# Optimization experiments

Measured on AMD Instinct MI355X. Metric: run time of the kernel, lower is better.

Reference implementation:

```python
import jax, jax.numpy as jnp
import numpy as np

B, C, H, W = 16, 192, 56, 56
WS = 7; L = WS * WS; NH = 8; HD = C // NH
SHIFTS = (0, 3, 0, 3)  # shift = 0 if i%2==0 else window_size//2


def _ln(x, g, b):
    m = jnp.mean(x, -1, keepdims=True)
    v = jnp.var(x, -1, keepdims=True)
    return (x - m) * jax.lax.rsqrt(v + 1e-5) * g + b


def _win_part(x):
    # (b, H, W, c) -> (b*nW, L, c)
    b, c = x.shape[0], x.shape[-1]
    x = x.reshape(b, H // WS, WS, W // WS, WS, c).transpose(0, 1, 3, 2, 4, 5)
    return x.reshape(-1, L, c)


def _win_rev(xw, b):
    # (b*nW, L, c) -> (b, H, W, c)
    c = xw.shape[-1]
    x = xw.reshape(b, H // WS, W // WS, WS, WS, c).transpose(0, 1, 3, 2, 4, 5)
    return x.reshape(b, H, W, c)


def _rel_index():
    co = np.stack(np.meshgrid(np.arange(WS), np.arange(WS), indexing='ij')).reshape(2, -1)
    r = (co[:, :, None] - co[:, None, :]).transpose(1, 2, 0).astype(np.int64)
    r[..., 0] += WS - 1; r[..., 1] += WS - 1; r[..., 0] *= 2 * WS - 1
    return r.sum(-1)  # (L, L)

REL_IDX = _rel_index()


def _mask(shift):
    if shift == 0:
        return None
    img = np.zeros((1, H, W, 1), np.float32)
    cnt = 0.0
    sl = (slice(0, H - WS), slice(H - WS, H - shift), slice(H - shift, None))
    for hs in sl:
        for ws_ in sl:
            img[:, hs, ws_, :] = cnt
            cnt += 1.0
    mw = np.asarray(_win_part(jnp.asarray(img))).reshape(-1, L)
    am = mw[:, None, :] - mw[:, :, None]
    return jnp.asarray(np.where(am != 0, -100.0, 0.0).astype(np.float32))  # (nW, L, L)

MASKS = [_mask(s) for s in SHIFTS]


def _block(x, n1g, n1b, qw, qb, pw, pb, tab, n2g, n2b, f1w, f1b, f2w, f2b, shift, mask):
    b = x.shape[0]
    sc = x
    x = _ln(x, n1g, n1b)
    if shift:
        x = jnp.roll(x, (-shift, -shift), (1, 2))
    xw = _win_part(x)  # (b*nW, L, C)
    qkv = (xw @ qw.T + qb).reshape(-1, L, 3, NH, HD).transpose(2, 0, 3, 1, 4)
    q, k, v = qkv[0], qkv[1], qkv[2]  # (nB, NH, L, HD)
    attn = jnp.einsum('bhid,bhjd->bhij', q * (HD ** -0.5), k)
    attn = attn + tab[REL_IDX].transpose(2, 0, 1)  # relative position bias (NH, L, L)
    if mask is not None:
        nW = mask.shape[0]
        attn = (attn.reshape(b, nW, NH, L, L) + mask[None, :, None]).reshape(-1, NH, L, L)
    attn = jax.nn.softmax(attn, -1)
    out = jnp.einsum('bhij,bhjd->bhid', attn, v).transpose(0, 2, 1, 3).reshape(-1, L, C)
    out = out @ pw.T + pb
    x = _win_rev(out, b)
    if shift:
        x = jnp.roll(x, (shift, shift), (1, 2))
    x = sc + x
    y = _ln(x, n2g, n2b)
    y = jax.nn.gelu(y @ f1w.T + f1b, approximate=False) @ f2w.T + f2b
    return x + y


def _conv_bn_relu(x, w, b, g, bt, m, v):
    x = jax.lax.conv_general_dilated(x, w, (1, 1), ((1, 1), (1, 1)),
                                     dimension_numbers=('NCHW', 'OIHW', 'NCHW'))
    x = x + b[None, :, None, None]
    x = (x - m[None, :, None, None]) * jax.lax.rsqrt(v + 1e-5)[None, :, None, None]
    x = x * g[None, :, None, None] + bt[None, :, None, None]
    return jax.nn.relu(x)


def setup_inputs() -> dict:
    key = jax.random.key(0)
    ks = iter(jax.random.split(key, 48))
    rn = lambda shape, s=0.02: jax.random.normal(next(ks), shape, jnp.float32) * s
    OD = 96
    return dict(
        x=jax.random.normal(next(ks), (B, C, H, W), jnp.float32),
        pos_embed=rn((1, H * W, C)),
        proj_w=rn((C, C)), proj_b=jnp.zeros((C,)),
        pe_g=jnp.ones((C,)), pe_b=jnp.zeros((C,)),
        n1_g=jnp.ones((4, C)), n1_b=jnp.zeros((4, C)),
        qkv_w=rn((4, 3 * C, C)), qkv_b=jnp.zeros((4, 3 * C)),
        attn_pw=rn((4, C, C)), attn_pb=jnp.zeros((4, C)),
        rel_tab=rn((4, (2 * WS - 1) ** 2, NH)),
        n2_g=jnp.ones((4, C)), n2_b=jnp.zeros((4, C)),
        fc1_w=rn((4, 4 * C, C)), fc1_b=jnp.zeros((4, 4 * C)),
        fc2_w=rn((4, C, 4 * C)), fc2_b=jnp.zeros((4, C)),
        c1_w=rn((C, C, 3, 3)), c1_b=jnp.zeros((C,)),
        bn1_g=jnp.ones((C,)), bn1_b=jnp.zeros((C,)), bn1_m=rn((C,), 0.1), bn1_v=jnp.ones((C,)),
        c2_w=rn((OD, C, 3, 3)), c2_b=jnp.zeros((OD,)),
        bn2_g=jnp.ones((OD,)), bn2_b=jnp.zeros((OD,)), bn2_m=rn((OD,), 0.1), bn2_v=jnp.ones((OD,)),
    )


def reference(x, pos_embed, proj_w, proj_b, pe_g, pe_b, n1_g, n1_b, qkv_w, qkv_b,
              attn_pw, attn_pb, rel_tab, n2_g, n2_b, fc1_w, fc1_b, fc2_w, fc2_b,
              c1_w, c1_b, bn1_g, bn1_b, bn1_m, bn1_v,
              c2_w, c2_b, bn2_g, bn2_b, bn2_m, bn2_v):
    # PatchEmbedding: 1x1 conv == per-pixel linear, then LN, + pos embed
    t = jnp.einsum('bchw,dc->bhwd', x, proj_w) + proj_b  # (B, H, W, D)
    t = _ln(t.reshape(B, H * W, C), pe_g, pe_b) + pos_embed
    o = t.reshape(B, H, W, C)
    for i in range(4):
        o = _block(o, n1_g[i], n1_b[i], qkv_w[i], qkv_b[i], attn_pw[i], attn_pb[i],
                   rel_tab[i], n2_g[i], n2_b[i], fc1_w[i], fc1_b[i], fc2_w[i], fc2_b[i],
                   SHIFTS[i], MASKS[i])
    ds2 = o.transpose(0, 3, 1, 2)  # (B, C, H, W)
    h1 = _conv_bn_relu(ds2, c1_w, c1_b, bn1_g, bn1_b, bn1_m, bn1_v)
    conv_out = _conv_bn_relu(h1, c2_w, c2_b, bn2_g, bn2_b, bn2_m, bn2_v)
    return (conv_out, ds2)
```

## Files before the change

kernel.cpp:

```cpp
#include <hip/hip_runtime.h>
#include <math.h>

typedef unsigned short u16;
typedef unsigned int u32;
typedef __attribute__((ext_vector_type(8))) short short8;
typedef __attribute__((ext_vector_type(4))) float f32x4;

#define IMG 56
#define HW_ 3136
#define NTOK 50176
#define C_DIM 192
#define CONV_OUT_SZ 4816896

#define SZ_QKV (4*576*192)
#define SZ_FC1 (4*768*192)
#define SZ_FC2 (4*192*768)
#define SZ_PW  (4*192*192)
#define SZ_PROJ (192*192)
#define SZ_C1R (192*1728)
#define SZ_C2R (128*1728)

__device__ inline float bf2f(u16 v) {
  u32 u = ((u32)v) << 16; float f; __builtin_memcpy(&f, &u, 4); return f;
}
__device__ inline u16 f2bf(float f) {
  u32 u; __builtin_memcpy(&u, &f, 4);
  u += 0x7FFF + ((u >> 16) & 1);
  return (u16)(u >> 16);
}
__device__ inline void glds16(const u16* g, u16* l) {
  __builtin_amdgcn_global_load_lds((const __attribute__((address_space(1))) u32*)g,
                                   (__attribute__((address_space(3))) u32*)l, 16, 0, 0);
}
__device__ inline u32 pk_bf16(float a, float b) {
  u32 r;
  asm("v_cvt_pk_bf16_f32 %0, %1, %2" : "=v"(r) : "v"(a), "v"(b));
  return r;
}

template<int AMODE, int EPI>
__global__ __launch_bounds__(256) void gmm(
    const u16* __restrict__ A, const u16* __restrict__ W,
    const float* __restrict__ bias, void* __restrict__ Cout,
    int M, int N, int K,
    const float* __restrict__ bg, const float* __restrict__ bb,
    const float* __restrict__ bm, const float* __restrict__ bv, int shiftp)
{
  __shared__ u16 As[128 * 64];
  __shared__ u16 Bs[64 * 64];
  const int tid = threadIdx.x;
  const int m0 = blockIdx.x * 128, n0 = blockIdx.y * 64;
  const int lane = tid & 63, wid = tid >> 6;
  const int wm = (wid >> 1) * 64, wn = (wid & 1) * 32;
  const int fr = lane & 15, fg = lane >> 4;
  f32x4 acc[4][2] = {};

  for (int kc = 0; kc < K; kc += 64) {
    #pragma unroll
    for (int it = 0; it < 2; ++it) {
      const int g = it * 256 + tid;
      const int row = g >> 3, cb = (g & 7) << 4;
      const int sc = cb ^ ((row & 7) << 4);
      glds16(W + (size_t)(n0 + row) * K + kc + (sc >> 1), Bs + g * 8);
    }
    if (AMODE == 0) {
      #pragma unroll
      for (int it = 0; it < 4; ++it) {
        const int g = it * 256 + tid;
        const int row = g >> 3, cb = (g & 7) << 4;
        const int sc = cb ^ ((row & 7) << 4);
        glds16(A + (size_t)(m0 + row) * K + kc + (sc >> 1), As + g * 8);
      }
    } else {
      #pragma unroll
      for (int it = 0; it < 4; ++it) {
        const int g = it * 256 + tid;
        const int row = g >> 3, cb = (g & 7) << 4;
        const int m = m0 + row;
        const int b = m / HW_, pp = m - b * HW_;
        const int y = pp / IMG, x = pp - (pp / IMG) * IMG;
        const int kg = kc + (cb >> 1);
        const int s = kg / C_DIM, ic = kg - s * C_DIM;
        const int yy = y + s / 3 - 1, xx = x + (s % 3) - 1;
        short8 v = {0, 0, 0, 0, 0, 0, 0, 0};
        if ((unsigned)yy < IMG && (unsigned)xx < IMG)
          v = *(const short8*)(A + ((size_t)(b * HW_ + yy * IMG + xx)) * C_DIM + ic);
        *(short8*)(As + row * 64 + ((cb ^ ((row & 7) << 4)) >> 1)) = v;
      }
    }
    __syncthreads();
    #pragma unroll
    for (int ks = 0; ks < 2; ++ks) {
      const int kb = ks * 64 + fg * 16;
      short8 af[4], bfv[2];
      #pragma unroll
      for (int i = 0; i < 4; ++i) {
        const int row = wm + i * 16 + fr;
        af[i] = *(const short8*)(As + ((row * 128 + (kb ^ ((row & 7) << 4))) >> 1));
      }
      #pragma unroll
      for (int j = 0; j < 2; ++j) {
        const int row = wn + j * 16 + fr;
        bfv[j] = *(const short8*)(Bs + ((row * 128 + (kb ^ ((row & 7) << 4))) >> 1));
      }
      #pragma unroll
      for (int i = 0; i < 4; ++i)
        #pragma unroll
        for (int j = 0; j < 2; ++j)
          acc[i][j] = __builtin_amdgcn_mfma_f32_16x16x32_bf16(af[i], bfv[j], acc[i][j], 0, 0, 0);
    }
    __syncthreads();
  }

  const int c0 = n0 + wn + fr;
  const int c1i = (EPI == 4) ? min(c0 + 16, N - 1) : (c0 + 16);
  const float bias0 = bias[c0], bias1 = bias[c1i];
  float s0 = 0.f, h0 = 0.f, s1 = 0.f, h1 = 0.f;
  if (EPI == 3 || EPI == 4) {
    s0 = bg[c0] * rsqrtf(bv[c0] + 1e-5f); h0 = bb[c0] - bm[c0] * s0;
    s1 = bg[c1i] * rsqrtf(bv[c1i] + 1e-5f); h1 = bb[c1i] - bm[c1i] * s1;
  }

  if (EPI == 0 || EPI == 1 || EPI == 3) {
    #pragma unroll
    for (int i = 0; i < 4; ++i) {
      #pragma unroll
      for (int r = 0; r < 4; ++r) {
        const int ml = wm + i * 16 + fg * 4 + r;
        #pragma unroll
        for (int j = 0; j < 2; ++j) {
          float v = acc[i][j][r] + (j ? bias1 : bias0);
          if (EPI == 1) v = 0.5f * v * (1.f + erff(v * 0.70710678118f));
          if (EPI == 3) { v = v * (j ? s1 : s0) + (j ? h1 : h0); v = fmaxf(v, 0.f); }
          const int cl = wn + j * 16 + fr;
          As[ml * 64 + ((cl & 7) | ((((cl >> 3) ^ ml) & 7) << 3))] = f2bf(v);
        }
      }
    }
    __syncthreads();
    #pragma unroll
    for (int p = 0; p < 4; ++p) {
      const int id = p * 256 + tid;
      const int ml = id >> 3, g = id & 7;
      const int pg = (g ^ ml) & 7;
      *(short8*)((u16*)Cout + (size_t)(m0 + ml) * N + n0 + g * 8) =
          *(const short8*)(As + ml * 64 + pg * 8);
    }
  } else {
    #pragma unroll
    for (int i = 0; i < 4; ++i) {
      #pragma unroll
      for (int r = 0; r < 4; ++r) {
        const int m = m0 + wm + i * 16 + fg * 4 + r;
        size_t sbase = 0;
        if (EPI == 6) {
          const int wno = m / 49, within = m - wno * 49;
          const int b2 = wno >> 6, wb3 = wno & 63;
          const int wr = within / 7, wc = within - wr * 7;
          int y2 = (wb3 >> 3) * 7 + wr + shiftp; if (y2 >= IMG) y2 -= IMG;
          int x2 = (wb3 & 7) * 7 + wc + shiftp; if (x2 >= IMG) x2 -= IMG;
          sbase = ((size_t)(b2 * HW_ + y2 * IMG + x2)) * C_DIM;
        }
        #pragma unroll
        for (int j = 0; j < 2; ++j) {
          const int c = c0 + j * 16;
          float v = acc[i][j][r] + (j ? bias1 : bias0);
          if (EPI == 4) { v = v * (j ? s1 : s0) + (j ? h1 : h0); v = fmaxf(v, 0.f); }
          if (EPI == 5) {
            ((float*)Cout)[(size_t)m * N + c] = v;
          } else if (EPI == 2) {
            ((float*)Cout)[(size_t)m * N + c] += v;
          } else if (EPI == 6) {
            ((float*)Cout)[sbase + c] += v;
          } else {
            if (c < N) {
              const int b = m / HW_, pp = m - b * HW_;
              ((float*)Cout)[((size_t)b * N + c) * HW_ + pp] = v;
            }
          }
        }
      }
    }
  }
}

__device__ inline void stv(float* p, float v) { *p = v; }
__device__ inline void stv(u16* p, float v) { *p = f2bf(v); }

template<typename OT>
__global__ __launch_bounds__(256) void ln_k(
    const float* __restrict__ in, OT* __restrict__ outp,
    const float* __restrict__ g, const float* __restrict__ bta,
    const float* __restrict__ pos, int winpart, int shift)
{
  const int t = blockIdx.x * 4 + (threadIdx.x >> 6);
  const int lane = threadIdx.x & 63;
  const float* xr = in + (size_t)t * C_DIM;
  const float v0 = xr[lane], v1 = xr[lane + 64], v2 = xr[lane + 128];
  float s = v0 + v1 + v2;
  float ss = v0 * v0 + v1 * v1 + v2 * v2;
  #pragma unroll
  for (int off = 32; off > 0; off >>= 1) {
    s += __shfl_xor(s, off);
    ss += __shfl_xor(ss, off);
  }
  const float mean = s * (1.f / 192.f);
  const float inv = rsqrtf(ss * (1.f / 192.f) - mean * mean + 1e-5f);
  const int b = t / HW_, pp = t - b * HW_;
  size_t obase;
  if (winpart) {
    const int y = pp / IMG, x = pp - (pp / IMG) * IMG;
    int yr = y - shift; if (yr < 0) yr += IMG;
    int xs = x - shift; if (xs < 0) xs += IMG;
    const int win = b * 64 + (yr / 7) * 8 + (xs / 7);
    const int within = (yr % 7) * 7 + (xs % 7);
    obase = ((size_t)win * 49 + within) * C_DIM;
  } else {
    obase = (size_t)t * C_DIM;
  }
  OT* o = outp + obase;
  float p0 = 0.f, p1 = 0.f, p2 = 0.f;
  if (pos) {
    const float* pr = pos + (size_t)pp * C_DIM;
    p0 = pr[lane]; p1 = pr[lane + 64]; p2 = pr[lane + 128];
  }
  stv(o + lane,       (v0 - mean) * inv * g[lane]       + bta[lane]       + p0);
  stv(o + lane + 64,  (v1 - mean) * inv * g[lane + 64]  + bta[lane + 64]  + p1);
  stv(o + lane + 128, (v2 - mean) * inv * g[lane + 128] + bta[lane + 128] + p2);
}

template<int SHIFT>
__global__ __launch_bounds__(256) void attn_m(
    const u16* __restrict__ qkv, u16* __restrict__ outp,
    const float* __restrict__ rel)
{
  __shared__ u16 VT[128 * 64];
  __shared__ float relS[4 * 176 + 16];
  const int tid = threadIdx.x;
  const int wid = tid >> 6, lane = tid & 63;
  const int fr = lane & 15, fg = lane >> 4;
  const int win = blockIdx.x >> 1;
  const int hb = blockIdx.x & 1;
  const int h = hb * 4 + wid;
  const u16* wbase = qkv + (size_t)win * 49 * 576;

  {
    u32* vz = (u32*)VT;
    #pragma unroll
    for (int it = 0; it < 16; ++it) vz[it * 256 + tid] = 0;
  }
  for (int id = tid; id < 169 * 4; id += 256) {
    const int hl = id & 3, ridx = id >> 2;
    relS[hl * 176 + ridx] = rel[ridx * 8 + hb * 4 + hl];
  }
  __syncthreads();
  for (int id = tid; id < 49 * 24; id += 256) {
    const int j = id / 24, dq = id - (id / 24) * 24;
    const int dd = dq * 4;
    const uint2 v = *(const uint2*)(wbase + j * 576 + 384 + hb * 96 + dd);
    const u16* pv = (const u16*)&v;
    const int wpr = dd / 24, dl = dd - wpr * 24;
    #pragma unroll
    for (int e = 0; e < 4; ++e) {
      const int row = wpr * 32 + dl + e;
      VT[(row * 128 + ((j * 2) ^ (((row >> 2) & 7) << 4))) >> 1] = pv[e];
    }
  }
  __syncthreads();

  short8 qf[4], kf[4];
  #pragma unroll
  for (int t = 0; t < 4; ++t) {
    const int row = t * 16 + fr;
    if (fg < 3) {
      qf[t] = *(const short8*)(wbase + row * 576 + h * 24 + fg * 8);
      kf[t] = *(const short8*)(wbase + row * 576 + 192 + h * 24 + fg * 8);
    } else {
      qf[t] = (short8){0, 0, 0, 0, 0, 0, 0, 0};
      kf[t] = (short8){0, 0, 0, 0, 0, 0, 0, 0};
    }
  }

  short8 av[2][2];
  #pragma unroll
  for (int db = 0; db < 2; ++db) {
    const int row = wid * 32 + db * 16 + fr;
    const int swz = ((row >> 2) & 7) << 4;
    #pragma unroll
    for (int ks = 0; ks < 2; ++ks) {
      const uint2 lo = *(const uint2*)((const char*)VT + row * 128 + (((2 * ks) * 32 + fg * 8) ^ swz));
      const uint2 hi = *(const uint2*)((const char*)VT + row * 128 + (((2 * ks + 1) * 32 + fg * 8) ^ swz));
      u32 w[4] = {lo.x, lo.y, hi.x, hi.y};
      av[db][ks] = *(short8*)w;
    }
  }

  const int wb2 = win & 63;
  const int hblk = wb2 >> 3, wblk = wb2 & 7;

  u32 joffPk[4];
  u32 jregPk[2] = {0, 0};
  #pragma unroll
  for (int nj = 0; nj < 4; ++nj) {
    u32 w = 0;
    #pragma unroll
    for (int r = 0; r < 4; ++r) {
      const int j = nj * 16 + fg * 4 + r;
      const int r2 = j / 7, c2 = j - r2 * 7;
      w |= (u32)(r2 * 13 + c2) << (r * 8);
      if (SHIFT) {
        const int hj = hblk * 7 + r2, wj = wblk * 7 + c2;
        const int rj = (hj < 49 ? 0 : (hj < 53 ? 1 : 2)) * 3 + (wj < 49 ? 0 : (wj < 53 ? 1 : 2));
        jregPk[nj >> 1] |= (u32)rj << (((nj & 1) * 4 + r) * 4);
      }
    }
    joffPk[nj] = w;
  }

  const float* relw = relS + wid * 176;
  const float scl = 0.20412414523193154f;

  #pragma unroll
  for (int mi = 0; mi < 4; ++mi) {
    f32x4 sacc[4];
    #pragma unroll
    for (int nj = 0; nj < 4; ++nj)
      sacc[nj] = __builtin_amdgcn_mfma_f32_16x16x32_bf16(kf[nj], qf[mi],
                                                         (f32x4){0, 0, 0, 0}, 0, 0, 0);
    const int i = mi * 16 + fr;
    const int r1 = i / 7, c1 = i - r1 * 7;
    const int base13 = (r1 + 6) * 13 + (c1 + 6);
    int ri = 0;
    if (SHIFT) {
      const int hi2 = hblk * 7 + r1, wi2 = wblk * 7 + c1;
      ri = (hi2 < 49 ? 0 : (hi2 < 53 ? 1 : 2)) * 3 + (wi2 < 49 ? 0 : (wi2 < 53 ? 1 : 2));
    }
    float p[16];
    float mx = -1e30f;
    #pragma unroll
    for (int nj = 0; nj < 4; ++nj) {
      #pragma unroll
      for (int r = 0; r < 4; ++r) {
        const int j = nj * 16 + fg * 4 + r;
        int idx = base13 - (int)((joffPk[nj] >> (r * 8)) & 0xff);
        idx = min(max(idx, 0), 168);
        float v = sacc[nj][r] * scl + relw[idx];
        if (SHIFT) {
          const int rj = (jregPk[nj >> 1] >> (((nj & 1) * 4 + r) * 4)) & 0xf;
          v = (ri != rj) ? v - 100.f : v;
        }
        v = (j < 49) ? v : -1e30f;
        p[nj * 4 + r] = v;
        mx = fmaxf(mx, v);
      }
    }
    mx = fmaxf(mx, __shfl_xor(mx, 16));
    mx = fmaxf(mx, __shfl_xor(mx, 32));
    float sum = 0.f;
    #pragma unroll
    for (int e = 0; e < 16; ++e) { p[e] = __expf(p[e] - mx); sum += p[e]; }
    sum += __shfl_xor(sum, 16);
    sum += __shfl_xor(sum, 32);
    const float inv = 1.f / sum;
    short8 pb[2];
    #pragma unroll
    for (int ks = 0; ks < 2; ++ks) {
      u32 w[4];
      #pragma unroll
      for (int half = 0; half < 2; ++half) {
        const int nj = 2 * ks + half;
        w[half * 2 + 0] = pk_bf16(p[nj * 4 + 0] * inv, p[nj * 4 + 1] * inv);
        w[half * 2 + 1] = pk_bf16(p[nj * 4 + 2] * inv, p[nj * 4 + 3] * inv);
      }
      pb[ks] = *(short8*)w;
    }
    f32x4 o0 = {0, 0, 0, 0}, o1 = {0, 0, 0, 0};
    o0 = __builtin_amdgcn_mfma_f32_16x16x32_bf16(av[0][0], pb[0], o0, 0, 0, 0);
    o0 = __builtin_amdgcn_mfma_f32_16x16x32_bf16(av[0][1], pb[1], o0, 0, 0, 0);
    o1 = __builtin_amdgcn_mfma_f32_16x16x32_bf16(av[1][0], pb[0], o1, 0, 0, 0);
    o1 = __builtin_amdgcn_mfma_f32_16x16x32_bf16(av[1][1], pb[1], o1, 0, 0, 0);
    if (i < 49) {
      u16* orow = outp + ((size_t)win * 49 + i) * C_DIM + h * 24;
      *(uint2*)(orow + fg * 4) =
          make_uint2(pk_bf16(o0[0], o0[1]), pk_bf16(o0[2], o0[3]));
      if (fg < 2)
        *(uint2*)(orow + 16 + fg * 4) =
            make_uint2(pk_bf16(o1[0], o1[1]), pk_bf16(o1[2], o1[3]));
    }
  }
}

__global__ __launch_bounds__(256) void transpose_k(
    const float* __restrict__ in, float* __restrict__ outp)
{
  __shared__ float tile[32][33];
  const int p0 = blockIdx.x * 32;
  const int c0 = blockIdx.y * 32;
  const int tid = threadIdx.x;
  #pragma unroll
  for (int it = 0; it < 4; ++it) {
    const int id = tid + it * 256;
    const int r = id >> 5, cc = id & 31;
    tile[r][cc] = in[(size_t)(p0 + r) * C_DIM + c0 + cc];
  }
  __syncthreads();
  const int b = p0 / HW_, pp0 = p0 - b * HW_;
  #pragma unroll
  for (int it = 0; it < 4; ++it) {
    const int id = tid + it * 256;
    const int cl = id >> 5, pl = id & 31;
    outp[((size_t)b * C_DIM + c0 + cl) * HW_ + pp0 + pl] = tile[pl][cl];
  }
}

__global__ __launch_bounds__(256) void tok_k(
    const float* __restrict__ in, u16* __restrict__ outp)
{
  __shared__ float tile[32][33];
  const int t0 = blockIdx.x * 32;
  const int c0 = blockIdx.y * 32;
  const int tid = threadIdx.x;
  const int b = t0 / HW_, p0 = t0 - b * HW_;
  #pragma unroll
  for (int it = 0; it < 4; ++it) {
    const int id = tid + it * 256;
    const int cl = id >> 5, pl = id & 31;
    tile[cl][pl] = in[((size_t)b * C_DIM + c0 + cl) * HW_ + p0 + pl];
  }
  __syncthreads();
  #pragma unroll
  for (int it = 0; it < 4; ++it) {
    const int id = tid + it * 256;
    const int r = id >> 5, cc = id & 31;
    outp[(size_t)(t0 + r) * C_DIM + c0 + cc] = f2bf(tile[cc][r]);
  }
}

__global__ __launch_bounds__(256) void cvt_k(
    const float* __restrict__ in, u16* __restrict__ outp, int n4)
{
  const int i = blockIdx.x * 256 + threadIdx.x;
  if (i >= n4) return;
  const float4 v = ((const float4*)in)[i];
  u32 lo = (u32)f2bf(v.x) | ((u32)f2bf(v.y) << 16);
  u32 hi = (u32)f2bf(v.z) | ((u32)f2bf(v.w) << 16);
  ((uint2*)outp)[i] = make_uint2(lo, hi);
}

__global__ __launch_bounds__(256) void cvtall_k(
    const float* __restrict__ qkv_w, const float* __restrict__ fc1_w,
    const float* __restrict__ fc2_w, const float* __restrict__ attn_pw,
    const float* __restrict__ proj_w, const float* __restrict__ c1_w,
    const float* __restrict__ c2_w, u16* __restrict__ wbf)
{
  const int i = blockIdx.x * 256 + threadIdx.x;
  const int off1 = SZ_QKV, off2 = off1 + SZ_FC1, off3 = off2 + SZ_FC2,
            off4 = off3 + SZ_PW, off5 = off4 + SZ_PROJ, off6 = off5 + SZ_C1R,
            off7 = off6 + SZ_C2R;
  if (i >= off7) return;
  float v;
  if (i < off1) v = qkv_w[i];
  else if (i < off2) v = fc1_w[i - off1];
  else if (i < off3) v = fc2_w[i - off2];
  else if (i < off4) v = attn_pw[i - off3];
  else if (i < off5) v = proj_w[i - off4];
  else if (i < off6) {
    const int e = i - off5;
    const int n = e / 1728, kkk = e - n * 1728;
    const int s = kkk / C_DIM, ic = kkk - s * C_DIM;
    v = c1_w[((size_t)n * C_DIM + ic) * 9 + s];
  } else {
    const int e = i - off6;
    const int n = e / 1728, kkk = e - n * 1728;
    const int s = kkk / C_DIM, ic = kkk - s * C_DIM;
    v = (n < 96) ? c2_w[((size_t)n * C_DIM + ic) * 9 + s] : 0.f;
  }
  wbf[i] = f2bf(v);
}

extern "C" void kernel_launch(void* const* d_in, const int* in_sizes, int n_in,
                              void* d_out, int out_size, void* d_ws, size_t ws_size,
                              hipStream_t stream)
{
  const float* x       = (const float*)d_in[0];
  const float* pos     = (const float*)d_in[1];
  const float* proj_w  = (const float*)d_in[2];
  const float* proj_b  = (const float*)d_in[3];
  const float* pe_g    = (const float*)d_in[4];
  const float* pe_b    = (const float*)d_in[5];
  const float* n1_g    = (const float*)d_in[6];
  const float* n1_b    = (const float*)d_in[7];
  const float* qkv_w   = (const float*)d_in[8];
  const float* qkv_b   = (const float*)d_in[9];
  const float* attn_pw = (const float*)d_in[10];
  const float* attn_pb = (const float*)d_in[11];
  const float* rel_tab = (const float*)d_in[12];
  const float* n2_g    = (const float*)d_in[13];
  const float* n2_b    = (const float*)d_in[14];
  const float* fc1_w   = (const float*)d_in[15];
  const float* fc1_b   = (const float*)d_in[16];
  const float* fc2_w   = (const float*)d_in[17];
  const float* fc2_b   = (const float*)d_in[18];
  const float* c1_w    = (const float*)d_in[19];
  const float* c1_b    = (const float*)d_in[20];
  const float* bn1_g   = (const float*)d_in[21];
  const float* bn1_b   = (const float*)d_in[22];
  const float* bn1_m   = (const float*)d_in[23];
  const float* bn1_v   = (const float*)d_in[24];
  const float* c2_w    = (const float*)d_in[25];
  const float* c2_b    = (const float*)d_in[26];
  const float* bn2_g   = (const float*)d_in[27];
  const float* bn2_b   = (const float*)d_in[28];
  const float* bn2_m   = (const float*)d_in[29];
  const float* bn2_v   = (const float*)d_in[30];
  float* out = (float*)d_out;

  const size_t BUF  = (size_t)NTOK * C_DIM * 4;
  const size_t BIGB = (size_t)NTOK * 576 * 2;
  char* ws = (char*)d_ws;
  float* act   = (float*)ws;
  u16*   big16 = (u16*)(ws + BUF);
  float* big32 = (float*)(ws + BUF);
  u16*   xln   = (u16*)(ws + BUF + BIGB);
  u16* attn_out = (u16*)d_out;
  u16* wbf = (u16*)((char*)d_out + (size_t)CONV_OUT_SZ * 4);

  const size_t O_QKV = 0;
  const size_t O_FC1 = O_QKV + SZ_QKV;
  const size_t O_FC2 = O_FC1 + SZ_FC1;
  const size_t O_PW  = O_FC2 + SZ_FC2;
  const size_t O_PROJ= O_PW  + SZ_PW;
  const size_t O_C1  = O_PROJ+ SZ_PROJ;
  const size_t O_C2  = O_C1  + SZ_C1R;

  const dim3 blk(256);

  const int cvtall_n = SZ_QKV + SZ_FC1 + SZ_FC2 + SZ_PW + SZ_PROJ + SZ_C1R + SZ_C2R;
  cvtall_k<<<(cvtall_n + 255) / 256, blk, 0, stream>>>(
      qkv_w, fc1_w, fc2_w, attn_pw, proj_w, c1_w, c2_w, wbf);

  tok_k<<<dim3(1568, 6), blk, 0, stream>>>(x, xln);
  gmm<0, 5><<<dim3(392, 3), blk, 0, stream>>>(
      xln, wbf + O_PROJ, proj_b, big32, NTOK, 192, 192,
      nullptr, nullptr, nullptr, nullptr, 0);
  ln_k<float><<<12544, blk, 0, stream>>>(big32, act, pe_g, pe_b, pos, 0, 0);

  for (int i = 0; i < 4; ++i) {
    const int shift = (i & 1) ? 3 : 0;
    ln_k<u16><<<12544, blk, 0, stream>>>(act, xln, n1_g + i * 192, n1_b + i * 192,
                                         nullptr, 1, shift);
    gmm<0, 0><<<dim3(392, 9), blk, 0, stream>>>(
        xln, wbf + O_QKV + (size_t)i * 576 * 192, qkv_b + i * 576, big16,
        NTOK, 576, 192, nullptr, nullptr, nullptr, nullptr, 0);
    if (shift)
      attn_m<3><<<2048, blk, 0, stream>>>(big16, attn_out, rel_tab + i * 169 * 8);
    else
      attn_m<0><<<2048, blk, 0, stream>>>(big16, attn_out, rel_tab + i * 169 * 8);
    gmm<0, 6><<<dim3(392, 3), blk, 0, stream>>>(
        attn_out, wbf + O_PW + (size_t)i * 192 * 192, attn_pb + i * 192, act,
        NTOK, 192, 192, nullptr, nullptr, nullptr, nullptr, shift);
    ln_k<u16><<<12544, blk, 0, stream>>>(act, xln, n2_g + i * 192, n2_b + i * 192,
                                         nullptr, 0, 0);
    for (int c = 0; c < 2; ++c) {
      gmm<0, 1><<<dim3(196, 12), blk, 0, stream>>>(
          xln + (size_t)c * 25088 * 192, wbf + O_FC1 + (size_t)i * 768 * 192,
          fc1_b + i * 768, big16, 25088, 768, 192,
          nullptr, nullptr, nullptr, nullptr, 0);
      gmm<0, 2><<<dim3(196, 3), blk, 0, stream>>>(
          big16, wbf + O_FC2 + (size_t)i * 192 * 768, fc2_b + i * 192,
          act + (size_t)c * 25088 * 192, 25088, 192, 768,
          nullptr, nullptr, nullptr, nullptr, 0);
    }
  }

  cvt_k<<<(NTOK * C_DIM / 4 + 255)/256, blk, 0, stream>>>(act, xln, NTOK * C_DIM / 4);
  gmm<1, 3><<<dim3(392, 3), blk, 0, stream>>>(
      xln, wbf + O_C1, c1_b, big16, NTOK, 192, 1728, bn1_g, bn1_b, bn1_m, bn1_v, 0);
  gmm<1, 4><<<dim3(392, 2), blk, 0, stream>>>(
      big16, wbf + O_C2, c2_b, out, NTOK, 96, 1728, bn2_g, bn2_b, bn2_m, bn2_v, 0);
  transpose_k<<<dim3(1568, 6), blk, 0, stream>>>(act, out + CONV_OUT_SZ);
}
```

Baseline: 962.3 us.

## Enlarge GEMM tile to 256x64 with each wave covering 64x64

The shared GEMM kernel's M tile grows from 128 to 256 rows. Each of the four waves now computes a 64x64 sub-tile (4x4 MFMA accumulators) instead of 64x32, so every B fragment loaded from LDS is reused across more MFMAs and the grid size is halved. The implicit-im2col conv loader is also split into batches of four global loads before the LDS stores, to put more loads in flight. In exchange the kernel uses more registers and LDS (which may lower occupancy) and launches fewer blocks, which may underfill the GPU for the smaller GEMMs.

```diff
diff --git a/kernel.cpp b/kernel.cpp
--- a/kernel.cpp
+++ b/kernel.cpp
@@ -46,14 +46,14 @@
     const float* __restrict__ bg, const float* __restrict__ bb,
     const float* __restrict__ bm, const float* __restrict__ bv, int shiftp)
 {
-  __shared__ u16 As[128 * 64];
+  __shared__ u16 As[256 * 64];
   __shared__ u16 Bs[64 * 64];
   const int tid = threadIdx.x;
-  const int m0 = blockIdx.x * 128, n0 = blockIdx.y * 64;
+  const int m0 = blockIdx.x * 256, n0 = blockIdx.y * 64;
   const int lane = tid & 63, wid = tid >> 6;
-  const int wm = (wid >> 1) * 64, wn = (wid & 1) * 32;
+  const int wm = wid * 64;
   const int fr = lane & 15, fg = lane >> 4;
-  f32x4 acc[4][2] = {};
+  f32x4 acc[4][4] = {};
 
   for (int kc = 0; kc < K; kc += 64) {
     #pragma unroll
@@ -65,7 +65,7 @@
     }
     if (AMODE == 0) {
       #pragma unroll
-      for (int it = 0; it < 4; ++it) {
+      for (int it = 0; it < 8; ++it) {
         const int g = it * 256 + tid;
         const int row = g >> 3, cb = (g & 7) << 4;
         const int sc = cb ^ ((row & 7) << 4);
@@ -73,52 +73,65 @@
       }
     } else {
       #pragma unroll
-      for (int it = 0; it < 4; ++it) {
-        const int g = it * 256 + tid;
-        const int row = g >> 3, cb = (g & 7) << 4;
-        const int m = m0 + row;
-        const int b = m / HW_, pp = m - b * HW_;
-        const int y = pp / IMG, x = pp - (pp / IMG) * IMG;
-        const int kg = kc + (cb >> 1);
-        const int s = kg / C_DIM, ic = kg - s * C_DIM;
-        const int yy = y + s / 3 - 1, xx = x + (s % 3) - 1;
-        short8 v = {0, 0, 0, 0, 0, 0, 0, 0};
-        if ((unsigned)yy < IMG && (unsigned)xx < IMG)
-          v = *(const short8*)(A + ((size_t)(b * HW_ + yy * IMG + xx)) * C_DIM + ic);
-        *(short8*)(As + row * 64 + ((cb ^ ((row & 7) << 4)) >> 1)) = v;
+      for (int half = 0; half < 2; ++half) {
+        short8 cst[4];
+        #pragma unroll
+        for (int it = 0; it < 4; ++it) {
+          const int g = (half * 4 + it) * 256 + tid;
+          const int row = g >> 3, cb = (g & 7) << 4;
+          const int m = m0 + row;
+          const int b = m / HW_, pp = m - b * HW_;
+          const int y = pp / IMG, x = pp - (pp / IMG) * IMG;
+          const int kg = kc + (cb >> 1);
+          const int s = kg / C_DIM, ic = kg - s * C_DIM;
+          const int yy = y + s / 3 - 1, xx = x + (s % 3) - 1;
+          short8 v = {0, 0, 0, 0, 0, 0, 0, 0};
+          if ((unsigned)yy < IMG && (unsigned)xx < IMG)
+            v = *(const short8*)(A + ((size_t)(b * HW_ + yy * IMG + xx)) * C_DIM + ic);
+          cst[it] = v;
+        }
+        #pragma unroll
+        for (int it = 0; it < 4; ++it) {
+          const int g = (half * 4 + it) * 256 + tid;
+          const int row = g >> 3, cb = (g & 7) << 4;
+          *(short8*)(As + row * 64 + ((cb ^ ((row & 7) << 4)) >> 1)) = cst[it];
+        }
       }
     }
     __syncthreads();
     #pragma unroll
     for (int ks = 0; ks < 2; ++ks) {
       const int kb = ks * 64 + fg * 16;
-      short8 af[4], bfv[2];
+      short8 af[4], bfv[4];
       #pragma unroll
       for (int i = 0; i < 4; ++i) {
         const int row = wm + i * 16 + fr;
         af[i] = *(const short8*)(As + ((row * 128 + (kb ^ ((row & 7) << 4))) >> 1));
       }
       #pragma unroll
-      for (int j = 0; j < 2; ++j) {
-        const int row = wn + j * 16 + fr;
+      for (int j = 0; j < 4; ++j) {
+        const int row = j * 16 + fr;
         bfv[j] = *(const short8*)(Bs + ((row * 128 + (kb ^ ((row & 7) << 4))) >> 1));
       }
       #pragma unroll
       for (int i = 0; i < 4; ++i)
         #pragma unroll
-        for (int j = 0; j < 2; ++j)
+        for (int j = 0; j < 4; ++j)
           acc[i][j] = __builtin_amdgcn_mfma_f32_16x16x32_bf16(af[i], bfv[j], acc[i][j], 0, 0, 0);
     }
     __syncthreads();
   }
 
-  const int c0 = n0 + wn + fr;
-  const int c1i = (EPI == 4) ? min(c0 + 16, N - 1) : (c0 + 16);
-  const float bias0 = bias[c0], bias1 = bias[c1i];
-  float s0 = 0.f, h0 = 0.f, s1 = 0.f, h1 = 0.f;
-  if (EPI == 3 || EPI == 4) {
-    s0 = bg[c0] * rsqrtf(bv[c0] + 1e-5f); h0 = bb[c0] - bm[c0] * s0;
-    s1 = bg[c1i] * rsqrtf(bv[c1i] + 1e-5f); h1 = bb[c1i] - bm[c1i] * s1;
+  const int c0 = n0 + fr;
+  float bias_[4], sc_[4], hh_[4];
+  #pragma unroll
+  for (int j = 0; j < 4; ++j) {
+    const int cj = (EPI == 4) ? min(c0 + j * 16, N - 1) : (c0 + j * 16);
+    bias_[j] = bias[cj];
+    if (EPI == 3 || EPI == 4) {
+      sc_[j] = bg[cj] * rsqrtf(bv[cj] + 1e-5f);
+      hh_[j] = bb[cj] - bm[cj] * sc_[j];
+    }
   }
 
   if (EPI == 0 || EPI == 1 || EPI == 3) {
@@ -128,18 +141,18 @@
       for (int r = 0; r < 4; ++r) {
         const int ml = wm + i * 16 + fg * 4 + r;
         #pragma unroll
-        for (int j = 0; j < 2; ++j) {
-          float v = acc[i][j][r] + (j ? bias1 : bias0);
+        for (int j = 0; j < 4; ++j) {
+          float v = acc[i][j][r] + bias_[j];
           if (EPI == 1) v = 0.5f * v * (1.f + erff(v * 0.70710678118f));
-          if (EPI == 3) { v = v * (j ? s1 : s0) + (j ? h1 : h0); v = fmaxf(v, 0.f); }
-          const int cl = wn + j * 16 + fr;
+          if (EPI == 3) { v = v * sc_[j] + hh_[j]; v = fmaxf(v, 0.f); }
+          const int cl = j * 16 + fr;
           As[ml * 64 + ((cl & 7) | ((((cl >> 3) ^ ml) & 7) << 3))] = f2bf(v);
         }
       }
     }
     __syncthreads();
     #pragma unroll
-    for (int p = 0; p < 4; ++p) {
+    for (int p = 0; p < 8; ++p) {
       const int id = p * 256 + tid;
       const int ml = id >> 3, g = id & 7;
       const int pg = (g ^ ml) & 7;
@@ -162,10 +175,10 @@
           sbase = ((size_t)(b2 * HW_ + y2 * IMG + x2)) * C_DIM;
         }
         #pragma unroll
-        for (int j = 0; j < 2; ++j) {
+        for (int j = 0; j < 4; ++j) {
           const int c = c0 + j * 16;
-          float v = acc[i][j][r] + (j ? bias1 : bias0);
-          if (EPI == 4) { v = v * (j ? s1 : s0) + (j ? h1 : h0); v = fmaxf(v, 0.f); }
+          float v = acc[i][j][r] + bias_[j];
+          if (EPI == 4) { v = v * sc_[j] + hh_[j]; v = fmaxf(v, 0.f); }
           if (EPI == 5) {
             ((float*)Cout)[(size_t)m * N + c] = v;
           } else if (EPI == 2) {
@@ -540,7 +553,7 @@
       qkv_w, fc1_w, fc2_w, attn_pw, proj_w, c1_w, c2_w, wbf);
 
   tok_k<<<dim3(1568, 6), blk, 0, stream>>>(x, xln);
-  gmm<0, 5><<<dim3(392, 3), blk, 0, stream>>>(
+  gmm<0, 5><<<dim3(196, 3), blk, 0, stream>>>(
       xln, wbf + O_PROJ, proj_b, big32, NTOK, 192, 192,
       nullptr, nullptr, nullptr, nullptr, 0);
   ln_k<float><<<12544, blk, 0, stream>>>(big32, act, pe_g, pe_b, pos, 0, 0);
@@ -549,24 +562,24 @@
     const int shift = (i & 1) ? 3 : 0;
     ln_k<u16><<<12544, blk, 0, stream>>>(act, xln, n1_g + i * 192, n1_b + i * 192,
                                          nullptr, 1, shift);
-    gmm<0, 0><<<dim3(392, 9), blk, 0, stream>>>(
+    gmm<0, 0><<<dim3(196, 9), blk, 0, stream>>>(
         xln, wbf + O_QKV + (size_t)i * 576 * 192, qkv_b + i * 576, big16,
         NTOK, 576, 192, nullptr, nullptr, nullptr, nullptr, 0);
     if (shift)
       attn_m<3><<<2048, blk, 0, stream>>>(big16, attn_out, rel_tab + i * 169 * 8);
     else
       attn_m<0><<<2048, blk, 0, stream>>>(big16, attn_out, rel_tab + i * 169 * 8);
-    gmm<0, 6><<<dim3(392, 3), blk, 0, stream>>>(
+    gmm<0, 6><<<dim3(196, 3), blk, 0, stream>>>(
         attn_out, wbf + O_PW + (size_t)i * 192 * 192, attn_pb + i * 192, act,
         NTOK, 192, 192, nullptr, nullptr, nullptr, nullptr, shift);
     ln_k<u16><<<12544, blk, 0, stream>>>(act, xln, n2_g + i * 192, n2_b + i * 192,
                                          nullptr, 0, 0);
     for (int c = 0; c < 2; ++c) {
-      gmm<0, 1><<<dim3(196, 12), blk, 0, stream>>>(
+      gmm<0, 1><<<dim3(98, 12), blk, 0, stream>>>(
           xln + (size_t)c * 25088 * 192, wbf + O_FC1 + (size_t)i * 768 * 192,
           fc1_b + i * 768, big16, 25088, 768, 192,
           nullptr, nullptr, nullptr, nullptr, 0);
-      gmm<0, 2><<<dim3(196, 3), blk, 0, stream>>>(
+      gmm<0, 2><<<dim3(98, 3), blk, 0, stream>>>(
           big16, wbf + O_FC2 + (size_t)i * 192 * 768, fc2_b + i * 192,
           act + (size_t)c * 25088 * 192, 25088, 192, 768,
           nullptr, nullptr, nullptr, nullptr, 0);
@@ -574,9 +587,9 @@
   }
 
   cvt_k<<<(NTOK * C_DIM / 4 + 255)/256, blk, 0, stream>>>(act, xln, NTOK * C_DIM / 4);
-  gmm<1, 3><<<dim3(392, 3), blk, 0, stream>>>(
+  gmm<1, 3><<<dim3(196, 3), blk, 0, stream>>>(
       xln, wbf + O_C1, c1_b, big16, NTOK, 192, 1728, bn1_g, bn1_b, bn1_m, bn1_v, 0);
-  gmm<1, 4><<<dim3(392, 2), blk, 0, stream>>>(
+  gmm<1, 4><<<dim3(196, 2), blk, 0, stream>>>(
       big16, wbf + O_C2, c2_b, out, NTOK, 96, 1728, bn2_g, bn2_b, bn2_m, bn2_v, 0);
   transpose_k<<<dim3(1568, 6), blk, 0, stream>>>(act, out + CONV_OUT_SZ);
 }
```

Result: slower. 1.163 ms (+20.9%).

## Store residual stream in bf16 and drop LDS-staged epilogue

Applied to the files above, without the earlier changes.

The residual activation buffer changes from fp32 to bf16. GEMM epilogues now read-modify-write bf16 directly, the layernorm reads bf16 with packed loads, and the final conversion kernel is removed because the conv GEMM consumes the activation directly. The aim is to halve the memory traffic of the residual stream across the many LN and GEMM passes. In exchange, residual accumulation loses precision, which risks exceeding the tolerance. The bf16 epilogue also switches from coalesced LDS-staged vector stores to scattered 2-byte scalar stores, which may hurt write efficiency.

```diff
diff --git a/kernel.cpp b/kernel.cpp
--- a/kernel.cpp
+++ b/kernel.cpp
@@ -120,63 +120,38 @@
     s0 = bg[c0] * rsqrtf(bv[c0] + 1e-5f); h0 = bb[c0] - bm[c0] * s0;
     s1 = bg[c1i] * rsqrtf(bv[c1i] + 1e-5f); h1 = bb[c1i] - bm[c1i] * s1;
   }
-
-  if (EPI == 0 || EPI == 1 || EPI == 3) {
-    #pragma unroll
-    for (int i = 0; i < 4; ++i) {
-      #pragma unroll
-      for (int r = 0; r < 4; ++r) {
-        const int ml = wm + i * 16 + fg * 4 + r;
-        #pragma unroll
-        for (int j = 0; j < 2; ++j) {
-          float v = acc[i][j][r] + (j ? bias1 : bias0);
-          if (EPI == 1) v = 0.5f * v * (1.f + erff(v * 0.70710678118f));
-          if (EPI == 3) { v = v * (j ? s1 : s0) + (j ? h1 : h0); v = fmaxf(v, 0.f); }
-          const int cl = wn + j * 16 + fr;
-          As[ml * 64 + ((cl & 7) | ((((cl >> 3) ^ ml) & 7) << 3))] = f2bf(v);
-        }
-      }
-    }
-    __syncthreads();
-    #pragma unroll
-    for (int p = 0; p < 4; ++p) {
-      const int id = p * 256 + tid;
-      const int ml = id >> 3, g = id & 7;
-      const int pg = (g ^ ml) & 7;
-      *(short8*)((u16*)Cout + (size_t)(m0 + ml) * N + n0 + g * 8) =
-          *(const short8*)(As + ml * 64 + pg * 8);
-    }
-  } else {
-    #pragma unroll
-    for (int i = 0; i < 4; ++i) {
-      #pragma unroll
-      for (int r = 0; r < 4; ++r) {
-        const int m = m0 + wm + i * 16 + fg * 4 + r;
-        size_t sbase = 0;
-        if (EPI == 6) {
-          const int wno = m / 49, within = m - wno * 49;
-          const int b2 = wno >> 6, wb3 = wno & 63;
-          const int wr = within / 7, wc = within - wr * 7;
-          int y2 = (wb3 >> 3) * 7 + wr + shiftp; if (y2 >= IMG) y2 -= IMG;
-          int x2 = (wb3 & 7) * 7 + wc + shiftp; if (x2 >= IMG) x2 -= IMG;
-          sbase = ((size_t)(b2 * HW_ + y2 * IMG + x2)) * C_DIM;
-        }
-        #pragma unroll
-        for (int j = 0; j < 2; ++j) {
-          const int c = c0 + j * 16;
-          float v = acc[i][j][r] + (j ? bias1 : bias0);
-          if (EPI == 4) { v = v * (j ? s1 : s0) + (j ? h1 : h0); v = fmaxf(v, 0.f); }
-          if (EPI == 5) {
-            ((float*)Cout)[(size_t)m * N + c] = v;
-          } else if (EPI == 2) {
-            ((float*)Cout)[(size_t)m * N + c] += v;
-          } else if (EPI == 6) {
-            ((float*)Cout)[sbase + c] += v;
-          } else {
-            if (c < N) {
-              const int b = m / HW_, pp = m - b * HW_;
-              ((float*)Cout)[((size_t)b * N + c) * HW_ + pp] = v;
-            }
+  #pragma unroll
+  for (int i = 0; i < 4; ++i) {
+    #pragma unroll
+    for (int r = 0; r < 4; ++r) {
+      const int m = m0 + wm + i * 16 + fg * 4 + r;
+      size_t sbase = 0;
+      if (EPI == 6) {
+        const int wno = m / 49, within = m - wno * 49;
+        const int b2 = wno >> 6, wb3 = wno & 63;
+        const int wr = within / 7, wc = within - wr * 7;
+        int y2 = (wb3 >> 3) * 7 + wr + shiftp; if (y2 >= IMG) y2 -= IMG;
+        int x2 = (wb3 & 7) * 7 + wc + shiftp; if (x2 >= IMG) x2 -= IMG;
+        sbase = ((size_t)(b2 * HW_ + y2 * IMG + x2)) * C_DIM;
+      }
+      #pragma unroll
+      for (int j = 0; j < 2; ++j) {
+        const int c = c0 + j * 16;
+        float v = acc[i][j][r] + (j ? bias1 : bias0);
+        if (EPI == 1) v = 0.5f * v * (1.f + erff(v * 0.70710678118f));
+        if (EPI == 3 || EPI == 4) { v = v * (j ? s1 : s0) + (j ? h1 : h0); v = fmaxf(v, 0.f); }
+        if (EPI == 0 || EPI == 1 || EPI == 3) {
+          ((u16*)Cout)[(size_t)m * N + c] = f2bf(v);
+        } else if (EPI == 2) {
+          u16* p = (u16*)Cout + (size_t)m * N + c;
+          *p = f2bf(bf2f(*p) + v);
+        } else if (EPI == 6) {
+          u16* p = (u16*)Cout + sbase + c;
+          *p = f2bf(bf2f(*p) + v);
+        } else {
+          if (c < N) {
+            const int b = m / HW_, pp = m - b * HW_;
+            ((float*)Cout)[((size_t)b * N + c) * HW_ + pp] = v;
           }
         }
       }
@@ -184,21 +159,20 @@
   }
 }
 
-__device__ inline void stv(float* p, float v) { *p = v; }
-__device__ inline void stv(u16* p, float v) { *p = f2bf(v); }
-
-template<typename OT>
 __global__ __launch_bounds__(256) void ln_k(
-    const float* __restrict__ in, OT* __restrict__ outp,
+    const u16* __restrict__ in, u16* __restrict__ outp,
     const float* __restrict__ g, const float* __restrict__ bta,
     const float* __restrict__ pos, int winpart, int shift)
 {
   const int t = blockIdx.x * 4 + (threadIdx.x >> 6);
   const int lane = threadIdx.x & 63;
-  const float* xr = in + (size_t)t * C_DIM;
-  const float v0 = xr[lane], v1 = xr[lane + 64], v2 = xr[lane + 128];
-  float s = v0 + v1 + v2;
-  float ss = v0 * v0 + v1 * v1 + v2 * v2;
+  const uint2* row = (const uint2*)(in + (size_t)t * C_DIM);
+  uint2 w = make_uint2(0, 0);
+  if (lane < 48) w = row[lane];
+  const float v0 = bf2f((u16)w.x), v1 = bf2f(w.x >> 16);
+  const float v2 = bf2f((u16)w.y), v3 = bf2f(w.y >> 16);
+  float s = v0 + v1 + v2 + v3;
+  float ss = v0 * v0 + v1 * v1 + v2 * v2 + v3 * v3;
   #pragma unroll
   for (int off = 32; off > 0; off >>= 1) {
     s += __shfl_xor(s, off);
@@ -218,15 +192,20 @@
   } else {
     obase = (size_t)t * C_DIM;
   }
-  OT* o = outp + obase;
-  float p0 = 0.f, p1 = 0.f, p2 = 0.f;
-  if (pos) {
-    const float* pr = pos + (size_t)pp * C_DIM;
-    p0 = pr[lane]; p1 = pr[lane + 64]; p2 = pr[lane + 128];
-  }
-  stv(o + lane,       (v0 - mean) * inv * g[lane]       + bta[lane]       + p0);
-  stv(o + lane + 64,  (v1 - mean) * inv * g[lane + 64]  + bta[lane + 64]  + p1);
-  stv(o + lane + 128, (v2 - mean) * inv * g[lane + 128] + bta[lane + 128] + p2);
+  if (lane < 48) {
+    const float4 gg = *(const float4*)(g + lane * 4);
+    const float4 bb = *(const float4*)(bta + lane * 4);
+    float p0 = 0.f, p1 = 0.f, p2 = 0.f, p3 = 0.f;
+    if (pos) {
+      const float4 pv = *(const float4*)(pos + (size_t)pp * C_DIM + lane * 4);
+      p0 = pv.x; p1 = pv.y; p2 = pv.z; p3 = pv.w;
+    }
+    const float r0 = (v0 - mean) * inv * gg.x + bb.x + p0;
+    const float r1 = (v1 - mean) * inv * gg.y + bb.y + p1;
+    const float r2 = (v2 - mean) * inv * gg.z + bb.z + p2;
+    const float r3 = (v3 - mean) * inv * gg.w + bb.w + p3;
+    ((uint2*)(outp + obase))[lane] = make_uint2(pk_bf16(r0, r1), pk_bf16(r2, r3));
+  }
 }
 
 template<int SHIFT>
@@ -391,17 +370,19 @@
 }
 
 __global__ __launch_bounds__(256) void transpose_k(
-    const float* __restrict__ in, float* __restrict__ outp)
+    const u16* __restrict__ in, float* __restrict__ outp)
 {
   __shared__ float tile[32][33];
   const int p0 = blockIdx.x * 32;
   const int c0 = blockIdx.y * 32;
   const int tid = threadIdx.x;
   #pragma unroll
-  for (int it = 0; it < 4; ++it) {
+  for (int it = 0; it < 2; ++it) {
     const int id = tid + it * 256;
-    const int r = id >> 5, cc = id & 31;
-    tile[r][cc] = in[(size_t)(p0 + r) * C_DIM + c0 + cc];
+    const int r = id >> 4, c2 = id & 15;
+    const u32 v = *(const u32*)(in + (size_t)(p0 + r) * C_DIM + c0 + c2 * 2);
+    tile[r][c2 * 2] = bf2f((u16)v);
+    tile[r][c2 * 2 + 1] = bf2f(v >> 16);
   }
   __syncthreads();
   const int b = p0 / HW_, pp0 = p0 - b * HW_;
@@ -434,17 +415,6 @@
     const int r = id >> 5, cc = id & 31;
     outp[(size_t)(t0 + r) * C_DIM + c0 + cc] = f2bf(tile[cc][r]);
   }
-}
-
-__global__ __launch_bounds__(256) void cvt_k(
-    const float* __restrict__ in, u16* __restrict__ outp, int n4)
-{
-  const int i = blockIdx.x * 256 + threadIdx.x;
-  if (i >= n4) return;
-  const float4 v = ((const float4*)in)[i];
-  u32 lo = (u32)f2bf(v.x) | ((u32)f2bf(v.y) << 16);
-  u32 hi = (u32)f2bf(v.z) | ((u32)f2bf(v.w) << 16);
-  ((uint2*)outp)[i] = make_uint2(lo, hi);
 }
 
 __global__ __launch_bounds__(256) void cvtall_k(
@@ -515,13 +485,12 @@
   const float* bn2_v   = (const float*)d_in[30];
   float* out = (float*)d_out;
 
-  const size_t BUF  = (size_t)NTOK * C_DIM * 4;
+  const size_t ACTB = (size_t)NTOK * C_DIM * 2;
   const size_t BIGB = (size_t)NTOK * 576 * 2;
   char* ws = (char*)d_ws;
-  float* act   = (float*)ws;
-  u16*   big16 = (u16*)(ws + BUF);
-  float* big32 = (float*)(ws + BUF);
-  u16*   xln   = (u16*)(ws + BUF + BIGB);
+  u16* act   = (u16*)ws;
+  u16* big16 = (u16*)(ws + ACTB);
+  u16* xln   = (u16*)(ws + ACTB + BIGB);
   u16* attn_out = (u16*)d_out;
   u16* wbf = (u16*)((char*)d_out + (size_t)CONV_OUT_SZ * 4);
 
@@ -540,15 +509,15 @@
       qkv_w, fc1_w, fc2_w, attn_pw, proj_w, c1_w, c2_w, wbf);
 
   tok_k<<<dim3(1568, 6), blk, 0, stream>>>(x, xln);
-  gmm<0, 5><<<dim3(392, 3), blk, 0, stream>>>(
-      xln, wbf + O_PROJ, proj_b, big32, NTOK, 192, 192,
+  gmm<0, 0><<<dim3(392, 3), blk, 0, stream>>>(
+      xln, wbf + O_PROJ, proj_b, big16, NTOK, 192, 192,
       nullptr, nullptr, nullptr, nullptr, 0);
-  ln_k<float><<<12544, blk, 0, stream>>>(big32, act, pe_g, pe_b, pos, 0, 0);
+  ln_k<<<12544, blk, 0, stream>>>(big16, act, pe_g, pe_b, pos, 0, 0);
 
   for (int i = 0; i < 4; ++i) {
     const int shift = (i & 1) ? 3 : 0;
-    ln_k<u16><<<12544, blk, 0, stream>>>(act, xln, n1_g + i * 192, n1_b + i * 192,
-                                         nullptr, 1, shift);
+    ln_k<<<12544, blk, 0, stream>>>(act, xln, n1_g + i * 192, n1_b + i * 192,
+                                    nullptr, 1, shift);
     gmm<0, 0><<<dim3(392, 9), blk, 0, stream>>>(
         xln, wbf + O_QKV + (size_t)i * 576 * 192, qkv_b + i * 576, big16,
         NTOK, 576, 192, nullptr, nullptr, nullptr, nullptr, 0);
@@ -559,8 +528,8 @@
     gmm<0, 6><<<dim3(392, 3), blk, 0, stream>>>(
         attn_out, wbf + O_PW + (size_t)i * 192 * 192, attn_pb + i * 192, act,
         NTOK, 192, 192, nullptr, nullptr, nullptr, nullptr, shift);
-    ln_k<u16><<<12544, blk, 0, stream>>>(act, xln, n2_g + i * 192, n2_b + i * 192,
-                                         nullptr, 0, 0);
+    ln_k<<<12544, blk, 0, stream>>>(act, xln, n2_g + i * 192, n2_b + i * 192,
+                                    nullptr, 0, 0);
     for (int c = 0; c < 2; ++c) {
       gmm<0, 1><<<dim3(196, 12), blk, 0, stream>>>(
           xln + (size_t)c * 25088 * 192, wbf + O_FC1 + (size_t)i * 768 * 192,
@@ -573,9 +542,8 @@
     }
   }
 
-  cvt_k<<<(NTOK * C_DIM / 4 + 255)/256, blk, 0, stream>>>(act, xln, NTOK * C_DIM / 4);
   gmm<1, 3><<<dim3(392, 3), blk, 0, stream>>>(
-      xln, wbf + O_C1, c1_b, big16, NTOK, 192, 1728, bn1_g, bn1_b, bn1_m, bn1_v, 0);
+      act, wbf + O_C1, c1_b, big16, NTOK, 192, 1728, bn1_g, bn1_b, bn1_m, bn1_v, 0);
   gmm<1, 4><<<dim3(392, 2), blk, 0, stream>>>(
       big16, wbf + O_C2, c2_b, out, NTOK, 96, 1728, bn2_g, bn2_b, bn2_m, bn2_v, 0);
   transpose_k<<<dim3(1568, 6), blk, 0, stream>>>(act, out + CONV_OUT_SZ);
```

After: 890.1 us. 1.08x faster.
